# Kernel tuning notes

Measured on AMD Instinct MI355X. Metric: run time of the kernel, lower is better.

## Reference

```python
import jax, jax.numpy as jnp
import numpy as np
import math

B, S, D = 4, 2048, 1024
TAU = 0.5

def setup_inputs() -> dict:
    key = jax.random.key(0)
    ks = jax.random.split(key, 10)
    s = 1.0 / math.sqrt(D)
    return {
        "node_emb": jax.random.normal(ks[0], (B, S, D), jnp.float32),
        "label_emb": jax.random.normal(ks[1], (B, S, D), jnp.float32),
        "Wq": jax.random.uniform(ks[2], (D, D), jnp.float32, -s, s),
        "bq": jax.random.uniform(ks[3], (D,), jnp.float32, -s, s),
        "Wk": jax.random.uniform(ks[4], (D, D), jnp.float32, -s, s),
        "bk": jax.random.uniform(ks[5], (D,), jnp.float32, -s, s),
        "Wv": jax.random.uniform(ks[6], (D, D), jnp.float32, -s, s),
        "bv": jax.random.uniform(ks[7], (D,), jnp.float32, -s, s),
        "Wp": jax.random.uniform(ks[8], (D, D), jnp.float32, -s, s),
        "bp": jax.random.uniform(ks[9], (D,), jnp.float32, -s, s),
    }

def reference(node_emb, label_emb, Wq, bq, Wk, bk, Wv, bv, Wp, bp):
    # Q from label_emb; K, V from node_emb (torch Linear: x @ W.T + b)
    Q = label_emb @ Wq.T + bq          # [B, S, D]
    K = node_emb @ Wk.T + bk           # [B, S, D]
    V = node_emb @ Wv.T + bv           # [B, S, D]
    d = node_emb.shape[-1]
    score = jnp.einsum('bqd,bkd->bqk', Q, K) / jnp.sqrt(jnp.float32(d))
    # causal (lower-triangular) mask, masked_fill(-1e9) BEFORE the tau scale
    causal = jnp.tril(jnp.ones((score.shape[-2], score.shape[-1]), bool))
    score = jnp.where(causal[None, :, :], score, jnp.float32(-1e9))
    attn = jax.nn.softmax(score * TAU, axis=-1)  # [B, S, S]
    # proj_drop is Dropout(0.1); reference runs in eval mode (identity)
    z = jnp.einsum('bqk,bkd->bqd', attn, V)
    return z @ Wp.T + bp
```

## Files before the change

kernel.cpp:

```cpp
#include <hip/hip_runtime.h>
#include <hip/hip_bf16.h>
#include <stdint.h>

using bf16 = __hip_bfloat16;
typedef __bf16 bf16x8 __attribute__((ext_vector_type(8)));
typedef float f32x4 __attribute__((ext_vector_type(4)));
typedef unsigned short u16x8 __attribute__((ext_vector_type(8)));
typedef unsigned short u16x4 __attribute__((ext_vector_type(4)));

#define AS1 __attribute__((address_space(1)))
#define AS3 __attribute__((address_space(3)))

__device__ inline unsigned short f2b(float f) {
    union { __hip_bfloat16 h; unsigned short u; } cv;
    cv.h = __float2bfloat16(f);
    return cv.u;
}

__global__ __launch_bounds__(256) void cvt_pair(const float* __restrict__ a, const float* __restrict__ b,
                                                u16x8* __restrict__ oa, u16x8* __restrict__ ob, long n8) {
    const float* in = blockIdx.y ? b : a;
    u16x8* out = blockIdx.y ? ob : oa;
    long i = (long)blockIdx.x * blockDim.x + threadIdx.x;
    const long stride = (long)gridDim.x * blockDim.x;
    const float4* in4 = (const float4*)in;
    for (; i < n8; i += stride) {
        float4 x = in4[2 * i], y = in4[2 * i + 1];
        u16x8 o;
        o[0] = f2b(x.x); o[1] = f2b(x.y); o[2] = f2b(x.z); o[3] = f2b(x.w);
        o[4] = f2b(y.x); o[5] = f2b(y.y); o[6] = f2b(y.z); o[7] = f2b(y.w);
        out[i] = o;
    }
}

__global__ __launch_bounds__(256) void cvt_quad(const float* __restrict__ a, const float* __restrict__ b,
                                                const float* __restrict__ c, const float* __restrict__ d,
                                                u16x8* __restrict__ oa, u16x8* __restrict__ ob,
                                                u16x8* __restrict__ oc, u16x8* __restrict__ od, long n8) {
    const int y = blockIdx.y;
    const float* in = y == 0 ? a : (y == 1 ? b : (y == 2 ? c : d));
    u16x8* out = y == 0 ? oa : (y == 1 ? ob : (y == 2 ? oc : od));
    long i = (long)blockIdx.x * blockDim.x + threadIdx.x;
    const long stride = (long)gridDim.x * blockDim.x;
    const float4* in4 = (const float4*)in;
    for (; i < n8; i += stride) {
        float4 x = in4[2 * i], z = in4[2 * i + 1];
        u16x8 o;
        o[0] = f2b(x.x); o[1] = f2b(x.y); o[2] = f2b(x.z); o[3] = f2b(x.w);
        o[4] = f2b(z.x); o[5] = f2b(z.y); o[6] = f2b(z.z); o[7] = f2b(z.w);
        out[i] = o;
    }
}

template <typename T> __device__ inline void storev(T* p, float v);
template <> __device__ inline void storev<float>(float* p, float v) { *p = v; }
template <> __device__ inline void storev<bf16>(bf16* p, float v) { *p = __float2bfloat16(v); }

template <typename OutT, int MODE, int BN>
__global__ __launch_bounds__(512, 2) void gemmX(
    const bf16* __restrict__ A0, const bf16* __restrict__ A1,
    const bf16* __restrict__ B0p, const bf16* __restrict__ B1p,
    OutT* __restrict__ C0, OutT* __restrict__ C1,
    const float* __restrict__ bias0, const float* __restrict__ bias1,
    float scale, int lda, int ldb, int ldc, int Kdim,
    long sA, long sB, long sC)
{
    constexpr int LDSZ = (BN == 256) ? 131072 : 98304;
    constexpr int BUFS = (BN == 256) ? 65536 : 49152;
    __shared__ __align__(16) char lds[LDSZ];

    const int nwg = gridDim.x;
    const int bid = blockIdx.x;
    const int s = (nwg & 7) ? bid : ((bid & 7) * (nwg >> 3) + (bid >> 3));

    int bm, ccol0, rowB0, seg = 0;
    const bf16 *A, *B;
    OutT* C;
    const float* bias = nullptr;

    if constexpr (MODE == 0) {
        bm = s >> 3; const int bnl = s & 7; seg = bnl >> 2;
        A = A0; B = B0p; rowB0 = bnl * 256;
        C = seg ? C1 : C0; bias = seg ? bias1 : bias0;
        ccol0 = (bnl & 3) * 256;
    } else if constexpr (MODE == 1) {
        seg = s >> 7; const int r = s & 127; bm = r >> 2; const int bn = r & 3;
        A = seg ? A1 : A0; B = seg ? B1p : B0p;
        C = seg ? C1 : C0; bias = seg ? nullptr : bias0;
        rowB0 = bn * 256; ccol0 = bn * 256;
    } else if constexpr (MODE == 2) {
        const int z = s / 36, f = s % 36;
        int m = 0;
        while ((m + 1) * (m + 2) / 2 <= f) ++m;
        bm = m; const int bn = f - m * (m + 1) / 2;
        A = A0 + (long)z * sA; B = B0p + (long)z * sB; C = C0 + (long)z * sC;
        rowB0 = bn * 256; ccol0 = bn * 256;
    } else {
        const int z = s >> 6, r = s & 63; bm = r >> 3; const int bn = r & 7;
        A = A0 + (long)z * sA; B = B0p + (long)z * sB; C = C0 + (long)z * sC;
        rowB0 = bn * 128; ccol0 = bn * 128; bias = bias0;
    }

    int KT = Kdim >> 6;
    if constexpr (MODE == 3) { const int lim = 4 * (bm + 1); if (lim < KT) KT = lim; }
    const int NIT = KT >> 1;

    const int tid = threadIdx.x;
    const int lane = tid & 63;
    const int w = tid >> 6;
    constexpr int WR = (BN == 256) ? 128 : 64;
    const int wm = (BN == 256) ? (w >> 2) : (w >> 1);
    const int wn = (BN == 256) ? (w & 3) : (w & 1);

    const int rowA0 = bm * 256;

    const int rr  = tid >> 3;
    const int lch = (tid & 7) ^ (rr & 7);
    const bf16* gAt = A + (long)(rowA0 + rr) * lda + lch * 8;
    const bf16* gBt = B + (long)(rowB0 + rr) * ldb + lch * 8;

#define LA(b) (lds + (b) * BUFS)
#define LB(b) (lds + 32768 + (b) * BUFS)

    auto SG2 = [&](const bf16* g, int ld, char* dst) {
        __builtin_amdgcn_global_load_lds((const AS1 void*)g,
            (AS3 void*)(dst + tid * 16), 16, 0, 0);
        __builtin_amdgcn_global_load_lds((const AS1 void*)(g + (long)64 * ld),
            (AS3 void*)(dst + 8192 + tid * 16), 16, 0, 0);
    };
    auto ST_A = [&](int kt, int half, int b) {
        SG2(gAt + (long)kt * 64 + (long)half * 128 * lda, lda, LA(b) + half * 16384);
    };
    auto ST_B = [&](int kt, int half, int b) {
        SG2(gBt + (long)kt * 64 + (long)half * 128 * ldb, ldb, LB(b) + half * 16384);
    };
    auto ST_B1 = [&](int kt, int b) {
        SG2(gBt + (long)kt * 64, ldb, LB(b));
    };

    const int abase = (wm * WR + (lane & 15)) * 128;
    const int bbase = (wn * 64 + (lane & 15)) * 128;
    const int cc0 = (((lane >> 4) << 4)) ^ ((lane & 7) << 4);
    const int cc1 = cc0 ^ 64;

#define RAF(b, mh, mi, kk) (*(const bf16x8*)(LA(b) + abase + (mh)*8192 + (mi)*2048 + ((kk) ? cc1 : cc0)))
#define RBF(b, ni, kk)     (*(const bf16x8*)(LB(b) + bbase + (ni)*2048 + ((kk) ? cc1 : cc0)))

    f32x4 acc[(BN == 256) ? 8 : 4][4] = {};
    bf16x8 ar[4][2], blo[2][2], bhi[2][2];

#define RD_A2(b, mh, MI0) { ar[MI0][0] = RAF(b, mh, MI0, 0); ar[MI0][1] = RAF(b, mh, MI0, 1); \
                            ar[(MI0)+1][0] = RAF(b, mh, (MI0)+1, 0); ar[(MI0)+1][1] = RAF(b, mh, (MI0)+1, 1); }
#define RD_BLO(b)   { blo[0][0] = RBF(b, 0, 0); blo[0][1] = RBF(b, 0, 1); blo[1][0] = RBF(b, 1, 0); blo[1][1] = RBF(b, 1, 1); }
#define RD_BHI(b)   { bhi[0][0] = RBF(b, 2, 0); bhi[0][1] = RBF(b, 2, 1); bhi[1][0] = RBF(b, 3, 0); bhi[1][1] = RBF(b, 3, 1); }

#define MQ1(MI, bb, MH, NB) { \
    f32x4 t0_ = acc[(MH)*4 + (MI)][(NB)]; \
    t0_ = __builtin_amdgcn_mfma_f32_16x16x32_bf16(ar[MI][0], bb[0][0], t0_, 0, 0, 0); \
    t0_ = __builtin_amdgcn_mfma_f32_16x16x32_bf16(ar[MI][1], bb[0][1], t0_, 0, 0, 0); \
    acc[(MH)*4 + (MI)][(NB)] = t0_; \
    f32x4 t1_ = acc[(MH)*4 + (MI)][(NB) + 1]; \
    t1_ = __builtin_amdgcn_mfma_f32_16x16x32_bf16(ar[MI][0], bb[1][0], t1_, 0, 0, 0); \
    t1_ = __builtin_amdgcn_mfma_f32_16x16x32_bf16(ar[MI][1], bb[1][1], t1_, 0, 0, 0); \
    acc[(MH)*4 + (MI)][(NB) + 1] = t1_; }

#define WAIT_LGKM0 { asm volatile("s_waitcnt lgkmcnt(0)" ::: "memory"); __builtin_amdgcn_sched_barrier(0); }
#define WAIT_LGKM4 { asm volatile("s_waitcnt lgkmcnt(4)" ::: "memory"); __builtin_amdgcn_sched_barrier(0); }
#define SCHEDB     __builtin_amdgcn_sched_barrier(0)

    auto BAR = [&]() { __builtin_amdgcn_s_barrier(); SCHEDB; };
    auto PRIO1 = [&]() { __builtin_amdgcn_s_setprio(1); };
    auto PRIO0 = [&]() { __builtin_amdgcn_s_setprio(0); };

    if constexpr (BN == 256) {
        ST_A(0, 0, 0); ST_A(0, 1, 0); ST_B(0, 0, 0); ST_B(0, 1, 0);
        ST_B(1, 0, 1); ST_B(1, 1, 1);
        asm volatile("s_waitcnt vmcnt(4)" ::: "memory");
        BAR();

        for (int i = 0; i < NIT; ++i) {
            const int t0 = 2 * i;
            const bool last = (i == NIT - 1);

            RD_BLO(0); RD_A2(0, 0, 0); SCHEDB; RD_A2(0, 0, 2);
            ST_A(t0 + 1, 0, 1);
            BAR(); WAIT_LGKM4; PRIO1();
            MQ1(0, blo, 0, 0); MQ1(1, blo, 0, 0);
            WAIT_LGKM0;
            MQ1(2, blo, 0, 0); MQ1(3, blo, 0, 0);
            PRIO0(); BAR();
            RD_BHI(0);
            ST_A(t0 + 1, 1, 1);
            BAR(); WAIT_LGKM0; PRIO1();
            MQ1(0, bhi, 0, 2); MQ1(1, bhi, 0, 2); MQ1(2, bhi, 0, 2); MQ1(3, bhi, 0, 2);
            PRIO0(); BAR();
            RD_A2(0, 1, 0); SCHEDB; RD_A2(0, 1, 2);
            if (!last) ST_B(t0 + 2, 0, 0);
            BAR(); WAIT_LGKM4; PRIO1();
            MQ1(0, bhi, 1, 2); MQ1(1, bhi, 1, 2);
            WAIT_LGKM0;
            MQ1(2, bhi, 1, 2); MQ1(3, bhi, 1, 2);
            PRIO0(); BAR();
            if (!last) { ST_B(t0 + 2, 1, 0);
                         asm volatile("s_waitcnt vmcnt(4)" ::: "memory"); }
            else       { asm volatile("s_waitcnt vmcnt(0)" ::: "memory"); }
            BAR(); WAIT_LGKM0; PRIO1();
            MQ1(0, blo, 1, 0); MQ1(1, blo, 1, 0); MQ1(2, blo, 1, 0); MQ1(3, blo, 1, 0);
            PRIO0(); BAR();
            RD_BLO(1); RD_A2(1, 0, 0); SCHEDB; RD_A2(1, 0, 2);
            if (!last) ST_A(t0 + 2, 0, 0);
            BAR(); WAIT_LGKM4; PRIO1();
            MQ1(0, blo, 0, 0); MQ1(1, blo, 0, 0);
            WAIT_LGKM0;
            MQ1(2, blo, 0, 0); MQ1(3, blo, 0, 0);
            PRIO0(); BAR();
            RD_BHI(1);
            if (!last) ST_A(t0 + 2, 1, 0);
            BAR(); WAIT_LGKM0; PRIO1();
            MQ1(0, bhi, 0, 2); MQ1(1, bhi, 0, 2); MQ1(2, bhi, 0, 2); MQ1(3, bhi, 0, 2);
            PRIO0(); BAR();
            RD_A2(1, 1, 0); SCHEDB; RD_A2(1, 1, 2);
            if (!last) ST_B(t0 + 3, 0, 1);
            BAR(); WAIT_LGKM4; PRIO1();
            MQ1(0, bhi, 1, 2); MQ1(1, bhi, 1, 2);
            WAIT_LGKM0;
            MQ1(2, bhi, 1, 2); MQ1(3, bhi, 1, 2);
            PRIO0(); BAR();
            if (!last) { ST_B(t0 + 3, 1, 1);
                         asm volatile("s_waitcnt vmcnt(4)" ::: "memory"); }
            BAR(); WAIT_LGKM0; PRIO1();
            MQ1(0, blo, 1, 0); MQ1(1, blo, 1, 0); MQ1(2, blo, 1, 0); MQ1(3, blo, 1, 0);
            PRIO0(); BAR();
        }
    } else {
        ST_A(0, 0, 0); ST_A(0, 1, 0); ST_B1(0, 0);
        ST_A(1, 0, 1); ST_A(1, 1, 1); ST_B1(1, 1);
        asm volatile("s_waitcnt vmcnt(6)" ::: "memory");
        BAR();

        for (int i = 0; i < NIT; ++i) {
            const int t0 = 2 * i;
            const bool last = (i == NIT - 1);

            RD_BLO(0); RD_A2(0, 0, 0); RD_A2(0, 0, 2); SCHEDB; RD_BHI(0);
            BAR(); WAIT_LGKM4; PRIO1();
            MQ1(0, blo, 0, 0); MQ1(1, blo, 0, 0); MQ1(2, blo, 0, 0); MQ1(3, blo, 0, 0);
            PRIO0(); BAR();
            if (!last) { ST_A(t0 + 2, 0, 0); ST_A(t0 + 2, 1, 0);
                         asm volatile("s_waitcnt vmcnt(4)" ::: "memory"); }
            else       { asm volatile("s_waitcnt vmcnt(0)" ::: "memory"); }
            BAR(); WAIT_LGKM0; PRIO1();
            MQ1(0, bhi, 0, 2); MQ1(1, bhi, 0, 2); MQ1(2, bhi, 0, 2); MQ1(3, bhi, 0, 2);
            PRIO0(); BAR();
            RD_BLO(1); RD_A2(1, 0, 0); RD_A2(1, 0, 2); SCHEDB; RD_BHI(1);
            if (!last) ST_B1(t0 + 2, 0);
            BAR(); WAIT_LGKM4; PRIO1();
            MQ1(0, blo, 0, 0); MQ1(1, blo, 0, 0); MQ1(2, blo, 0, 0); MQ1(3, blo, 0, 0);
            PRIO0(); BAR();
            if (!last) { ST_A(t0 + 3, 0, 1); ST_A(t0 + 3, 1, 1); ST_B1(t0 + 3, 1);
                         asm volatile("s_waitcnt vmcnt(6)" ::: "memory"); }
            BAR(); WAIT_LGKM0; PRIO1();
            MQ1(0, bhi, 0, 2); MQ1(1, bhi, 0, 2); MQ1(2, bhi, 0, 2); MQ1(3, bhi, 0, 2);
            PRIO0(); BAR();
        }
    }

    constexpr int MF = (BN == 256) ? 8 : 4;
    if (MODE == 1 && seg == 1) {
        const int m0 = rowA0 + wm * WR + ((lane >> 4) << 2);
        const int z2 = m0 >> 11;
        const int lr0 = m0 & 2047;
        bf16* CT = (bf16*)C + (long)z2 * 2097152;
#pragma unroll
        for (int ni = 0; ni < 4; ++ni) {
            const int c = ccol0 + wn * 64 + (lane & 15) + ni * 16;
#pragma unroll
            for (int mi = 0; mi < MF; ++mi) {
                u16x4 o;
                o[0] = f2b(acc[mi][ni][0]); o[1] = f2b(acc[mi][ni][1]);
                o[2] = f2b(acc[mi][ni][2]); o[3] = f2b(acc[mi][ni][3]);
                *(u16x4*)(CT + (long)c * 2048 + lr0 + mi * 16) = o;
            }
        }
    } else {
        const int r0 = rowA0 + wm * WR + ((lane >> 4) << 2);
        const int c0 = ccol0 + wn * 64 + (lane & 15);
        const bool HB = (bias != nullptr);
#pragma unroll
        for (int ni = 0; ni < 4; ++ni) {
            const int c = c0 + ni * 16;
            const float bv = HB ? bias[c] : 0.0f;
#pragma unroll
            for (int mi = 0; mi < MF; ++mi) {
#pragma unroll
                for (int j = 0; j < 4; ++j) {
                    const long r = r0 + mi * 16 + j;
                    storev<OutT>(&C[r * (long)ldc + c], acc[mi][ni][j] * scale + bv);
                }
            }
        }
    }
#undef RAF
#undef RBF
#undef RD_A2
#undef RD_BLO
#undef RD_BHI
#undef MQ1
#undef LA
#undef LB
}

__global__ __launch_bounds__(256) void softmax_causal(bf16* __restrict__ SP, int S) {
    const int i = blockIdx.x;
    bf16* row = SP + ((long)blockIdx.y * S + i) * (long)S;
    const int L = i + 1;
    const int tid = threadIdx.x;
    const int lane = tid & 63, wid = tid >> 6;

    float v[8];
    int nv = 0;
    float m = -3.0e38f;
    for (int j = tid; j < L; j += 256) {
        float x = __bfloat162float(row[j]);
        v[nv++] = x;
        m = fmaxf(m, x);
    }
#pragma unroll
    for (int d = 32; d; d >>= 1) m = fmaxf(m, __shfl_xor(m, d));
    __shared__ float redm[4], reds[4];
    if (lane == 0) redm[wid] = m;
    __syncthreads();
    m = fmaxf(fmaxf(redm[0], redm[1]), fmaxf(redm[2], redm[3]));

    float ssum = 0.f;
    for (int t = 0; t < nv; ++t) { v[t] = __expf(v[t] - m); ssum += v[t]; }
#pragma unroll
    for (int d = 32; d; d >>= 1) ssum += __shfl_xor(ssum, d);
    if (lane == 0) reds[wid] = ssum;
    __syncthreads();
    ssum = reds[0] + reds[1] + reds[2] + reds[3];
    const float inv = 1.0f / ssum;

    nv = 0;
    for (int j = tid; j < L; j += 256) row[j] = __float2bfloat16(v[nv++] * inv);
    const int Lpad = ((i >> 8) + 1) << 8;
    for (int j = L + tid; j < Lpad; j += 256) row[j] = __float2bfloat16(0.0f);
}

extern "C" void kernel_launch(void* const* d_in, const int* in_sizes, int n_in,
                              void* d_out, int out_size, void* d_ws, size_t ws_size,
                              hipStream_t stream) {
    const int B = 4, S = 2048, D = 1024;
    const long MD = (long)B * S * D;
    const float scale = 0.5f / 32.0f;

    const float* node  = (const float*)d_in[0];
    const float* label = (const float*)d_in[1];
    const float* Wq = (const float*)d_in[2];
    const float* bq = (const float*)d_in[3];
    const float* Wk = (const float*)d_in[4];
    const float* bk = (const float*)d_in[5];
    const float* Wv = (const float*)d_in[6];
    const float* bv = (const float*)d_in[7];
    const float* Wp = (const float*)d_in[8];
    const float* bp = (const float*)d_in[9];
    float* out = (float*)d_out;

    char* ws = (char*)d_ws;
    bf16* nodeb  = (bf16*)(ws);
    bf16* VTb    = nodeb;
    bf16* labelb = (bf16*)(ws + 16777216);
    bf16* Wqb = (bf16*)(ws + 33554432);
    bf16* Wkb = (bf16*)(ws + 35651584);
    bf16* Wvb = (bf16*)(ws + 37748736);
    bf16* Wpb = (bf16*)(ws + 39845888);
    bf16* Qb  = (bf16*)(ws + 41943040);
    bf16* Kb  = (bf16*)(ws + 58720256);
    bf16* Vb  = (bf16*)(ws + 75497472);
    bf16* SP  = (bf16*)(ws + 92274688);
    if (ws_size < 125829120UL) return;

    dim3 blk(256);

    cvt_pair<<<dim3(512, 2), blk, 0, stream>>>(node, label, (u16x8*)nodeb, (u16x8*)labelb, MD / 8);
    cvt_quad<<<dim3(64, 4), blk, 0, stream>>>(Wq, Wk, Wv, Wp,
        (u16x8*)Wqb, (u16x8*)Wkb, (u16x8*)Wvb, (u16x8*)Wpb, (long)D * D / 8);

    gemmX<bf16, 0, 256><<<256, 512, 0, stream>>>(
        nodeb, nullptr, Wkb, nullptr, Kb, Vb, bk, bv,
        1.0f, D, D, D, D, 0, 0, 0);

    gemmX<bf16, 1, 256><<<256, 512, 0, stream>>>(
        labelb, Vb, Wqb, Wpb, Qb, VTb, bq, nullptr,
        1.0f, D, D, D, D, 0, 0, 0);

    gemmX<bf16, 2, 256><<<144, 512, 0, stream>>>(
        Qb, nullptr, Kb, nullptr, SP, nullptr, nullptr, nullptr,
        scale, D, D, S, D, (long)S * D, (long)S * D, (long)S * S);

    softmax_causal<<<dim3(S, B), blk, 0, stream>>>(SP, S);

    gemmX<float, 3, 128><<<256, 512, 0, stream>>>(
        SP, nullptr, VTb, nullptr, out, nullptr, bp, nullptr,
        1.0f, S, S, D, S, (long)S * S, (long)D * S, (long)S * D);
}
```

Before: 187.4 us.

## Merge GEMM pipeline phases and stage transposed epilogue through LDS

The BN=256 main loop is restructured from eight barrier-separated phases into four. Each phase now issues both A or B half-tile loads and the bhi fragment reads up front and waits on lgkmcnt(8), which removes half the barriers and priority toggles. The transposed bf16 epilogue (MODE 1, seg 1) now writes accumulators into a per-wave swizzled LDS buffer, then reads them back so each lane stores contiguous 16-byte rows to global memory instead of scattered 8-byte stores. This raises register and LDS live ranges per phase and assumes the LDS region is free and large enough after the loop, with no barrier before reuse.

```diff
diff --git a/kernel.cpp b/kernel.cpp
--- a/kernel.cpp
+++ b/kernel.cpp
@@ -166,6 +166,7 @@
 
 #define WAIT_LGKM0 { asm volatile("s_waitcnt lgkmcnt(0)" ::: "memory"); __builtin_amdgcn_sched_barrier(0); }
 #define WAIT_LGKM4 { asm volatile("s_waitcnt lgkmcnt(4)" ::: "memory"); __builtin_amdgcn_sched_barrier(0); }
+#define WAIT_LGKM8 { asm volatile("s_waitcnt lgkmcnt(8)" ::: "memory"); __builtin_amdgcn_sched_barrier(0); }
 #define SCHEDB     __builtin_amdgcn_sched_barrier(0)
 
     auto BAR = [&]() { __builtin_amdgcn_s_barrier(); SCHEDB; };
@@ -182,53 +183,42 @@
             const int t0 = 2 * i;
             const bool last = (i == NIT - 1);
 
-            RD_BLO(0); RD_A2(0, 0, 0); SCHEDB; RD_A2(0, 0, 2);
-            ST_A(t0 + 1, 0, 1);
-            BAR(); WAIT_LGKM4; PRIO1();
+            RD_BLO(0); RD_A2(0, 0, 0); SCHEDB; RD_A2(0, 0, 2); RD_BHI(0);
+            ST_A(t0 + 1, 0, 1); ST_A(t0 + 1, 1, 1);
+            BAR(); WAIT_LGKM8; PRIO1();
             MQ1(0, blo, 0, 0); MQ1(1, blo, 0, 0);
             WAIT_LGKM0;
             MQ1(2, blo, 0, 0); MQ1(3, blo, 0, 0);
-            PRIO0(); BAR();
-            RD_BHI(0);
-            ST_A(t0 + 1, 1, 1);
-            BAR(); WAIT_LGKM0; PRIO1();
             MQ1(0, bhi, 0, 2); MQ1(1, bhi, 0, 2); MQ1(2, bhi, 0, 2); MQ1(3, bhi, 0, 2);
             PRIO0(); BAR();
+
             RD_A2(0, 1, 0); SCHEDB; RD_A2(0, 1, 2);
-            if (!last) ST_B(t0 + 2, 0, 0);
+            if (!last) { ST_B(t0 + 2, 0, 0); ST_B(t0 + 2, 1, 0);
+                         asm volatile("s_waitcnt vmcnt(4)" ::: "memory"); }
+            else       { asm volatile("s_waitcnt vmcnt(0)" ::: "memory"); }
             BAR(); WAIT_LGKM4; PRIO1();
             MQ1(0, bhi, 1, 2); MQ1(1, bhi, 1, 2);
             WAIT_LGKM0;
             MQ1(2, bhi, 1, 2); MQ1(3, bhi, 1, 2);
-            PRIO0(); BAR();
-            if (!last) { ST_B(t0 + 2, 1, 0);
-                         asm volatile("s_waitcnt vmcnt(4)" ::: "memory"); }
-            else       { asm volatile("s_waitcnt vmcnt(0)" ::: "memory"); }
-            BAR(); WAIT_LGKM0; PRIO1();
             MQ1(0, blo, 1, 0); MQ1(1, blo, 1, 0); MQ1(2, blo, 1, 0); MQ1(3, blo, 1, 0);
             PRIO0(); BAR();
-            RD_BLO(1); RD_A2(1, 0, 0); SCHEDB; RD_A2(1, 0, 2);
-            if (!last) ST_A(t0 + 2, 0, 0);
-            BAR(); WAIT_LGKM4; PRIO1();
+
+            RD_BLO(1); RD_A2(1, 0, 0); SCHEDB; RD_A2(1, 0, 2); RD_BHI(1);
+            if (!last) { ST_A(t0 + 2, 0, 0); ST_A(t0 + 2, 1, 0); }
+            BAR(); WAIT_LGKM8; PRIO1();
             MQ1(0, blo, 0, 0); MQ1(1, blo, 0, 0);
             WAIT_LGKM0;
             MQ1(2, blo, 0, 0); MQ1(3, blo, 0, 0);
-            PRIO0(); BAR();
-            RD_BHI(1);
-            if (!last) ST_A(t0 + 2, 1, 0);
-            BAR(); WAIT_LGKM0; PRIO1();
             MQ1(0, bhi, 0, 2); MQ1(1, bhi, 0, 2); MQ1(2, bhi, 0, 2); MQ1(3, bhi, 0, 2);
             PRIO0(); BAR();
+
             RD_A2(1, 1, 0); SCHEDB; RD_A2(1, 1, 2);
-            if (!last) ST_B(t0 + 3, 0, 1);
+            if (!last) { ST_B(t0 + 3, 0, 1); ST_B(t0 + 3, 1, 1);
+                         asm volatile("s_waitcnt vmcnt(4)" ::: "memory"); }
             BAR(); WAIT_LGKM4; PRIO1();
             MQ1(0, bhi, 1, 2); MQ1(1, bhi, 1, 2);
             WAIT_LGKM0;
             MQ1(2, bhi, 1, 2); MQ1(3, bhi, 1, 2);
-            PRIO0(); BAR();
-            if (!last) { ST_B(t0 + 3, 1, 1);
-                         asm volatile("s_waitcnt vmcnt(4)" ::: "memory"); }
-            BAR(); WAIT_LGKM0; PRIO1();
             MQ1(0, blo, 1, 0); MQ1(1, blo, 1, 0); MQ1(2, blo, 1, 0); MQ1(3, blo, 1, 0);
             PRIO0(); BAR();
         }
@@ -246,17 +236,20 @@
             BAR(); WAIT_LGKM4; PRIO1();
             MQ1(0, blo, 0, 0); MQ1(1, blo, 0, 0); MQ1(2, blo, 0, 0); MQ1(3, blo, 0, 0);
             PRIO0(); BAR();
+
             if (!last) { ST_A(t0 + 2, 0, 0); ST_A(t0 + 2, 1, 0);
                          asm volatile("s_waitcnt vmcnt(4)" ::: "memory"); }
             else       { asm volatile("s_waitcnt vmcnt(0)" ::: "memory"); }
             BAR(); WAIT_LGKM0; PRIO1();
             MQ1(0, bhi, 0, 2); MQ1(1, bhi, 0, 2); MQ1(2, bhi, 0, 2); MQ1(3, bhi, 0, 2);
             PRIO0(); BAR();
+
             RD_BLO(1); RD_A2(1, 0, 0); RD_A2(1, 0, 2); SCHEDB; RD_BHI(1);
             if (!last) ST_B1(t0 + 2, 0);
             BAR(); WAIT_LGKM4; PRIO1();
             MQ1(0, blo, 0, 0); MQ1(1, blo, 0, 0); MQ1(2, blo, 0, 0); MQ1(3, blo, 0, 0);
             PRIO0(); BAR();
+
             if (!last) { ST_A(t0 + 3, 0, 1); ST_A(t0 + 3, 1, 1); ST_B1(t0 + 3, 1);
                          asm volatile("s_waitcnt vmcnt(6)" ::: "memory"); }
             BAR(); WAIT_LGKM0; PRIO1();
@@ -267,20 +260,31 @@
 
     constexpr int MF = (BN == 256) ? 8 : 4;
     if (MODE == 1 && seg == 1) {
-        const int m0 = rowA0 + wm * WR + ((lane >> 4) << 2);
-        const int z2 = m0 >> 11;
-        const int lr0 = m0 & 2047;
-        bf16* CT = (bf16*)C + (long)z2 * 2097152;
+        char* tw = lds + w * 16384;
 #pragma unroll
         for (int ni = 0; ni < 4; ++ni) {
-            const int c = ccol0 + wn * 64 + (lane & 15) + ni * 16;
-#pragma unroll
-            for (int mi = 0; mi < MF; ++mi) {
+            const int cl = ni * 16 + (lane & 15);
+            const int sw = 8 * (cl & 7);
+#pragma unroll
+            for (int mi = 0; mi < 8; ++mi) {
+                const int rlb = mi * 16 + ((lane >> 4) << 2);
                 u16x4 o;
                 o[0] = f2b(acc[mi][ni][0]); o[1] = f2b(acc[mi][ni][1]);
                 o[2] = f2b(acc[mi][ni][2]); o[3] = f2b(acc[mi][ni][3]);
-                *(u16x4*)(CT + (long)c * 2048 + lr0 + mi * 16) = o;
+                *(u16x4*)(tw + cl * 256 + 2 * (rlb ^ sw)) = o;
             }
+        }
+        asm volatile("s_waitcnt lgkmcnt(0)" ::: "memory");
+        __builtin_amdgcn_sched_barrier(0);
+        const int m0 = rowA0 + wm * 128;
+        const int z2 = m0 >> 11, mr = m0 & 2047;
+        bf16* CT = (bf16*)C + (long)z2 * 2097152 + (long)(ccol0 + wn * 64 + lane) * 2048 + mr;
+        const char* tr = tw + lane * 256;
+        const int sw2 = lane & 7;
+#pragma unroll
+        for (int rb = 0; rb < 16; ++rb) {
+            u16x8 v = *(const u16x8*)(tr + 16 * (rb ^ sw2));
+            *(u16x8*)(CT + 8 * rb) = v;
         }
     } else {
         const int r0 = rowA0 + wm * WR + ((lane >> 4) << 2);
```

New measurement: 193.1 us. 3.1% more time.
